# Kernel optimization log

Hardware: AMD Instinct MI355X
Metric: run time of the kernel (lower is better)

## Reference

```python
import jax, jax.numpy as jnp
import numpy as np
import math

N, T, NS, NO, HID = 256, 1000, 10, 10, 64


def gru_seq(x, Wi, Wh, bi, bh):
    # x: [N,T,D] -> hidden states [N,T,HID] (single-layer GRU, h0 = 0)
    xproj = x @ Wi + bi  # [N,T,3H], precompute input projections
    def step(h, xp):
        hp = h @ Wh + bh
        xr, xz, xn = jnp.split(xp, 3, axis=-1)
        hr, hz, hn = jnp.split(hp, 3, axis=-1)
        r = jax.nn.sigmoid(xr + hr)
        z = jax.nn.sigmoid(xz + hz)
        n = jnp.tanh(xn + r * hn)
        h_new = (1.0 - z) * n + z * h
        return h_new, h_new
    h0 = jnp.zeros((x.shape[0], Wh.shape[0]), x.dtype)
    _, hs = jax.lax.scan(step, h0, jnp.swapaxes(xproj, 0, 1))
    return jnp.swapaxes(hs, 0, 1)


def setup_inputs() -> dict:
    key = jax.random.key(0)
    ks = jax.random.split(key, 12)
    D = NO + NS  # GRU input = concat(y, x_hat)
    s = lambda fan: 1.0 / np.sqrt(fan)
    inp = {
        "Yi_batch": jax.random.normal(ks[0], (N, T, NO), jnp.float32),
        "X_hat_batch": jax.random.normal(ks[1], (N, T, NS), jnp.float32),
        # per-sample observation noise covariance: 0.5*I plus small random diagonal
        "Cw_batch": 0.5 * jnp.eye(NO, dtype=jnp.float32)[None] + jnp.eye(NO)[None] * 0.1 * jax.random.uniform(ks[2], (N, 1, 1), jnp.float32),
        "H": jax.random.normal(ks[3], (NO, NS), jnp.float32) * s(NS),
        "mu_w": jnp.zeros((NO, 1), jnp.float32),
        "Wi": jax.random.normal(ks[4], (D, 3 * HID), jnp.float32) * s(D),
        "Wh": jax.random.normal(ks[5], (HID, 3 * HID), jnp.float32) * s(HID),
        "bi": jnp.zeros((3 * HID,), jnp.float32),
        "bh": jnp.zeros((3 * HID,), jnp.float32),
        "W_mu": jax.random.normal(ks[6], (HID, NS), jnp.float32) * s(HID),
        "b_mu": jnp.zeros((NS,), jnp.float32),
        "W_var": jax.random.normal(ks[7], (HID, NS), jnp.float32) * s(HID),
        "b_var": jnp.zeros((NS,), jnp.float32),
    }
    return inp


def reference(Yi_batch, X_hat_batch, Cw_batch, H, mu_w, Wi, Wh, bi, bh, W_mu, b_mu, W_var, b_var):
    n_obs = Yi_batch.shape[-1]
    Tlen = Yi_batch.shape[1]
    # RNN: mu and (positive) vars per time step
    hs = gru_seq(jnp.concatenate([Yi_batch, X_hat_batch], axis=-1), Wi, Wh, bi, bh)
    mu_prev = hs @ W_mu + b_mu                       # [N,T,NS]
    var_prev = jax.nn.softplus(hs @ W_var + b_var)   # [N,T,NS] diag of L_xt_yt_prev
    # marginal over y: mu_y = H mu_prev + mu_w ; L_y = H diag(var) H^T + Cw
    mu_y = jnp.einsum('ij,ntj->nti', H, mu_prev) + mu_w[:, 0]
    HLH = jnp.einsum('ij,ntj,kj->ntik', H, var_prev, H)   # [N,T,NO,NO]
    L_y = HLH + Cw_batch[:, None]                          # broadcast Cw over time
    e = Yi_batch - mu_y
    # Gaussian log-likelihood via Cholesky (L_y is SPD)
    chol = jnp.linalg.cholesky(L_y)
    logdet = 2.0 * jnp.sum(jnp.log(jnp.diagonal(chol, axis1=-2, axis2=-1)), axis=-1)  # [N,T]
    sol = jnp.linalg.solve(L_y, e[..., None])[..., 0]
    quad = jnp.sum(e * sol, axis=-1)                       # [N,T]
    logprob = (-0.5 * n_obs * Tlen * math.log(2.0 * math.pi)
               - 0.5 * jnp.sum(logdet, axis=1)
               - 0.5 * jnp.sum(quad, axis=1))              # [N]
    return jnp.mean(logprob / (Tlen * n_obs))
```

## Files before the change

kernel.cpp:

```cpp
#include <hip/hip_runtime.h>
#include <math.h>

#define BN 256
#define TT 1000
#define NO 10
#define NS 10
#define HID 64
#define DIN 20
#define G3 192
#define WV 4
#define KW 16
#define GS 8
#define NG 125

__device__ __forceinline__ float bcast(float v, int l) {
    return __int_as_float(__builtin_amdgcn_readlane(__float_as_int(v), l));
}
__device__ __forceinline__ float rcpf(float x) { return __builtin_amdgcn_rcpf(x); }

__device__ __forceinline__ void sync_lds() {
    asm volatile("s_waitcnt lgkmcnt(0)\n\ts_barrier" ::: "memory");
}

__global__
__attribute__((amdgpu_flat_work_group_size(256, 256), amdgpu_waves_per_eu(1, 1)))
void gru_phase1(const float* __restrict__ Yi, const float* __restrict__ Xh,
                const float* __restrict__ Wi, const float* __restrict__ Wh,
                const float* __restrict__ bi, const float* __restrict__ bh,
                const float* __restrict__ Wmu, const float* __restrict__ Wvar,
                float* __restrict__ mv_out) {
    const int tid = threadIdx.x;
    const int lane = tid & 63;
    const int w = tid >> 6;
    const int kb = w * KW;

    __shared__ float4 part[2][WV][HID];
    __shared__ float pamv[2][WV][HID];
    __shared__ float inbuf[2][GS * DIN];
    __shared__ float obuf[2][GS * DIN];

    const int n = blockIdx.x;
    const float* ybase = Yi + (size_t)n * TT * NO;
    const float* xbase = Xh + (size_t)n * TT * NS;
    float* obase = mv_out + (size_t)n * TT * DIN;

    float whr[KW], whz[KW], whn[KW], wmv[KW];
    float wir[5], wiz[5], win[5];
#pragma unroll
    for (int k = 0; k < KW; ++k) {
        const int kk = kb + k;
        whr[k] = Wh[kk * G3 + lane];
        whz[k] = Wh[kk * G3 + 64 + lane];
        whn[k] = Wh[kk * G3 + 128 + lane];
        float wm = (lane < NS) ? Wmu[kk * NS + lane] : 0.0f;
        float wv = (lane >= NS && lane < 2 * NS) ? Wvar[kk * NS + (lane - NS)] : 0.0f;
        wmv[k] = wm + wv;
    }
#pragma unroll
    for (int k = 0; k < 5; ++k) {
        const int d = 5 * w + k;
        wir[k] = Wi[d * G3 + lane];
        wiz[k] = Wi[d * G3 + 64 + lane];
        win[k] = Wi[d * G3 + 128 + lane];
    }
    const float b_r  = bi[lane] + bh[lane];
    const float b_z  = bi[64 + lane] + bh[64 + lane];
    const float bx_n = bi[128 + lane];
    const float bh_n = bh[128 + lane];

    const int ibase = ((w >= 2) ? 80 : 0) + (w & 1) * 5;

    if (tid < 160)
        inbuf[0][tid] = (tid < 80) ? ybase[tid] : xbase[tid - 80];
    sync_lds();

    float h = 0.0f;

#pragma unroll 1
    for (int g = 0; g < NG; ++g) {
        float ld = 0.0f;
        const bool do_ld = (tid < 160) && (g + 1 < NG);
        if (do_ld)
            ld = (tid < 80) ? ybase[(size_t)(g + 1) * 80 + tid]
                            : xbase[(size_t)(g + 1) * 80 + (tid - 80)];
        const float* ib = inbuf[g & 1];

#pragma unroll
        for (int s = 0; s < GS; ++s) {
            const int ro = ibase + 10 * s;
            const float x0 = ib[ro], x1 = ib[ro + 1], x2 = ib[ro + 2];
            const float x3 = ib[ro + 3], x4 = ib[ro + 4];
            float pr = x0 * wir[0], pz = x0 * wiz[0], px = x0 * win[0];
            pr = fmaf(x1, wir[1], pr); pz = fmaf(x1, wiz[1], pz); px = fmaf(x1, win[1], px);
            pr = fmaf(x2, wir[2], pr); pz = fmaf(x2, wiz[2], pz); px = fmaf(x2, win[2], px);
            pr = fmaf(x3, wir[3], pr); pz = fmaf(x3, wiz[3], pz); px = fmaf(x3, win[3], px);
            pr = fmaf(x4, wir[4], pr); pz = fmaf(x4, wiz[4], pz); px = fmaf(x4, win[4], px);
            float pn = 0.0f, pm = 0.0f;
#pragma unroll
            for (int k = 0; k < KW; ++k) {
                float sv = bcast(h, kb + k);
                pr = fmaf(sv, whr[k], pr);
                pz = fmaf(sv, whz[k], pz);
                pn = fmaf(sv, whn[k], pn);
                pm = fmaf(sv, wmv[k], pm);
            }
            const int bufp = s & 1;
            part[bufp][w][lane] = make_float4(pr, pz, px, pn);
            pamv[bufp][w][lane] = pm;
            if (s == GS - 1 && do_ld) inbuf[(g + 1) & 1][tid] = ld;
            sync_lds();

            const float4 q0 = part[bufp][0][lane];
            const float4 q1 = part[bufp][1][lane];
            const float4 q2 = part[bufp][2][lane];
            const float4 q3 = part[bufp][3][lane];
            const float ar = b_r  + ((q0.x + q1.x) + (q2.x + q3.x));
            const float az = b_z  + ((q0.y + q1.y) + (q2.y + q3.y));
            const float ax = bx_n + ((q0.z + q1.z) + (q2.z + q3.z));
            const float ah = bh_n + ((q0.w + q1.w) + (q2.w + q3.w));
            if (w == 3) {
                float amv = (pamv[bufp][0][lane] + pamv[bufp][1][lane])
                          + (pamv[bufp][2][lane] + pamv[bufp][3][lane]);
                if (lane < DIN && !(g == 0 && s == 0)) {
                    const int tm1 = 8 * g + s - 1;
                    obuf[(tm1 >> 3) & 1][(tm1 & 7) * DIN + lane] = amv;
                }
            }
            if (s == 1 && g >= 1 && tid < 160)
                obase[(size_t)(g - 1) * 160 + tid] = obuf[(g - 1) & 1][tid];

            float r = rcpf(1.0f + __expf(-ar));
            float z = rcpf(1.0f + __expf(-az));
            float pre = fmaf(r, ah, ax);
            float e2 = __expf(2.0f * pre);
            float nn = 1.0f - 2.0f * rcpf(e2 + 1.0f);
            h = fmaf(z, h - nn, nn);
        }
    }

    {
        float pm = 0.0f;
#pragma unroll
        for (int k = 0; k < KW; ++k) pm = fmaf(bcast(h, kb + k), wmv[k], pm);
        pamv[0][w][lane] = pm;
        sync_lds();
        if (w == 3 && lane < DIN) {
            float amv = (pamv[0][0][lane] + pamv[0][1][lane])
                      + (pamv[0][2][lane] + pamv[0][3][lane]);
            obuf[0][7 * DIN + lane] = amv;
        }
        sync_lds();
        if (tid < 160)
            obase[(size_t)(NG - 1) * 160 + tid] = obuf[0][tid];
    }
}

__global__ void init_out(float* out) {
    out[0] = -0.918938533204672742f;
}

__global__ __launch_bounds__(256)
void lik_phase2(const float* __restrict__ Yi, const float* __restrict__ Cw,
                const float* __restrict__ Hm, const float* __restrict__ mu_w,
                const float* __restrict__ b_mu, const float* __restrict__ b_var,
                const float* __restrict__ mv_in, float* __restrict__ out) {
    __shared__ float sH[NO * NS];
    __shared__ float smw[NO], sbm[NS], sbv[NS];
    __shared__ float ssum[4];
    const int tid = threadIdx.x;
    if (tid < NO * NS) sH[tid] = Hm[tid];
    if (tid < NO) smw[tid] = mu_w[tid];
    if (tid < NS) { sbm[tid] = b_mu[tid]; sbv[tid] = b_var[tid]; }
    __syncthreads();

    const int gid = blockIdx.x * 256 + tid;
    float contrib = 0.0f;
    if (gid < BN * TT) {
        const int n = gid / TT;
        const float* mv = mv_in + (size_t)gid * DIN;
        float mu[NS], va[NS];
#pragma unroll
        for (int i = 0; i < NS; ++i) {
            mu[i] = mv[i] + sbm[i];
            float x = mv[NS + i] + sbv[i];
            va[i] = (x > 0.0f) ? (x + log1pf(__expf(-x))) : log1pf(__expf(x));
        }
        const float* y = Yi + (size_t)gid * NO;
        float e[NO];
#pragma unroll
        for (int i = 0; i < NO; ++i) {
            float m = smw[i];
#pragma unroll
            for (int j = 0; j < NS; ++j) m = fmaf(sH[i * NS + j], mu[j], m);
            e[i] = y[i] - m;
        }
        float M[NO][NO];
        const float* cw = Cw + (size_t)n * NO * NO;
#pragma unroll
        for (int i = 0; i < NO; ++i)
#pragma unroll
            for (int j = 0; j <= i; ++j) M[i][j] = cw[i * NO + j];
#pragma unroll
        for (int l = 0; l < NS; ++l) {
            float vl = va[l];
            float hv[NO];
#pragma unroll
            for (int i = 0; i < NO; ++i) hv[i] = sH[i * NS + l];
#pragma unroll
            for (int i = 0; i < NO; ++i) {
                float hvi = hv[i] * vl;
#pragma unroll
                for (int j = 0; j <= i; ++j) M[i][j] = fmaf(hvi, hv[j], M[i][j]);
            }
        }
        float logdet = 0.0f;
        float drs[NO];
#pragma unroll
        for (int j = 0; j < NO; ++j) {
            float d = M[j][j];
#pragma unroll
            for (int k = 0; k < j; ++k) d = fmaf(-M[j][k], M[j][k], d);
            logdet += __logf(d);
            float rs = __frsqrt_rn(d);
            drs[j] = rs;
            M[j][j] = d * rs;
#pragma unroll
            for (int i = j + 1; i < NO; ++i) {
                float v = M[i][j];
#pragma unroll
                for (int k = 0; k < j; ++k) v = fmaf(-M[i][k], M[j][k], v);
                M[i][j] = v * rs;
            }
        }
        float wv[NO];
        float quad = 0.0f;
#pragma unroll
        for (int i = 0; i < NO; ++i) {
            float v = e[i];
#pragma unroll
            for (int k = 0; k < i; ++k) v = fmaf(-M[i][k], wv[k], v);
            wv[i] = v * drs[i] * rcpf(M[i][i] * drs[i]);
            quad = fmaf(wv[i], wv[i], quad);
        }
        const float SCALE = 0.5f / ((float)BN * (float)TT * (float)NO);
        contrib = -(logdet + quad) * SCALE;
    }

#pragma unroll
    for (int off = 32; off > 0; off >>= 1) contrib += __shfl_down(contrib, off);
    if ((tid & 63) == 0) ssum[tid >> 6] = contrib;
    __syncthreads();
    if (tid == 0) {
        float s = ssum[0] + ssum[1] + ssum[2] + ssum[3];
        atomicAdd(out, s);
    }
}

extern "C" void kernel_launch(void* const* d_in, const int* in_sizes, int n_in,
                              void* d_out, int out_size, void* d_ws, size_t ws_size,
                              hipStream_t stream) {
    const float* Yi    = (const float*)d_in[0];
    const float* Xh    = (const float*)d_in[1];
    const float* Cw    = (const float*)d_in[2];
    const float* Hm    = (const float*)d_in[3];
    const float* mu_w  = (const float*)d_in[4];
    const float* Wi    = (const float*)d_in[5];
    const float* Wh    = (const float*)d_in[6];
    const float* bi    = (const float*)d_in[7];
    const float* bh    = (const float*)d_in[8];
    const float* W_mu  = (const float*)d_in[9];
    const float* b_mu  = (const float*)d_in[10];
    const float* W_var = (const float*)d_in[11];
    const float* b_var = (const float*)d_in[12];
    float* out = (float*)d_out;
    float* mv  = (float*)d_ws;

    init_out<<<1, 1, 0, stream>>>(out);
    gru_phase1<<<dim3(BN), dim3(256), 0, stream>>>(Yi, Xh, Wi, Wh, bi, bh,
                                                   W_mu, W_var, mv);
    lik_phase2<<<dim3((BN * TT + 255) / 256), dim3(256), 0, stream>>>(
        Yi, Cw, Hm, mu_w, b_mu, b_var, mv, out);
}
```

Baseline: 593.6 us.

## Run each GRU sample on a single wavefront with full hidden weights in registers

Replaces the four-wave-per-sample GRU kernel with one 64-lane wave per sample. Each wave holds all 64 recurrent weight rows plus the input weights in registers, so the per-step cross-wave LDS reduction and workgroup barrier go away. Inputs are staged through a per-wave LDS buffer in a padded interleaved layout, and outputs are written straight to global memory each step. In exchange each wave does four times the FMAs and readlanes per step on one SIMD, and register pressure rises to roughly 320 VGPRs.

Measured after the change: 1.064 ms. 1.79x slower.

```diff
diff --git a/kernel.cpp b/kernel.cpp
--- a/kernel.cpp
+++ b/kernel.cpp
@@ -8,8 +8,6 @@
 #define HID 64
 #define DIN 20
 #define G3 192
-#define WV 4
-#define KW 16
 #define GS 8
 #define NG 125
 
@@ -18,140 +16,112 @@
 }
 __device__ __forceinline__ float rcpf(float x) { return __builtin_amdgcn_rcpf(x); }
 
-__device__ __forceinline__ void sync_lds() {
-    asm volatile("s_waitcnt lgkmcnt(0)\n\ts_barrier" ::: "memory");
-}
-
 __global__
-__attribute__((amdgpu_flat_work_group_size(256, 256), amdgpu_waves_per_eu(1, 1)))
-void gru_phase1(const float* __restrict__ Yi, const float* __restrict__ Xh,
-                const float* __restrict__ Wi, const float* __restrict__ Wh,
-                const float* __restrict__ bi, const float* __restrict__ bh,
-                const float* __restrict__ Wmu, const float* __restrict__ Wvar,
-                float* __restrict__ mv_out) {
-    const int tid = threadIdx.x;
-    const int lane = tid & 63;
-    const int w = tid >> 6;
-    const int kb = w * KW;
-
-    __shared__ float4 part[2][WV][HID];
-    __shared__ float pamv[2][WV][HID];
-    __shared__ float inbuf[2][GS * DIN];
-    __shared__ float obuf[2][GS * DIN];
-
+__attribute__((amdgpu_flat_work_group_size(64, 64), amdgpu_waves_per_eu(1, 1)))
+void gru_onewave(const float* __restrict__ Yi, const float* __restrict__ Xh,
+                 const float* __restrict__ Wi, const float* __restrict__ Wh,
+                 const float* __restrict__ bi, const float* __restrict__ bh,
+                 const float* __restrict__ Wmu, const float* __restrict__ Wvar,
+                 float* __restrict__ mv_out) {
+    const int lane = threadIdx.x;
     const int n = blockIdx.x;
-    const float* ybase = Yi + (size_t)n * TT * NO;
-    const float* xbase = Xh + (size_t)n * TT * NS;
-    float* obase = mv_out + (size_t)n * TT * DIN;
-
-    float whr[KW], whz[KW], whn[KW], wmv[KW];
-    float wir[5], wiz[5], win[5];
-#pragma unroll
-    for (int k = 0; k < KW; ++k) {
-        const int kk = kb + k;
-        whr[k] = Wh[kk * G3 + lane];
-        whz[k] = Wh[kk * G3 + 64 + lane];
-        whn[k] = Wh[kk * G3 + 128 + lane];
-        float wm = (lane < NS) ? Wmu[kk * NS + lane] : 0.0f;
-        float wv = (lane >= NS && lane < 2 * NS) ? Wvar[kk * NS + (lane - NS)] : 0.0f;
-        wmv[k] = wm + wv;
-    }
-#pragma unroll
-    for (int k = 0; k < 5; ++k) {
-        const int d = 5 * w + k;
-        wir[k] = Wi[d * G3 + lane];
-        wiz[k] = Wi[d * G3 + 64 + lane];
-        win[k] = Wi[d * G3 + 128 + lane];
-    }
-    const float b_r  = bi[lane] + bh[lane];
-    const float b_z  = bi[64 + lane] + bh[64 + lane];
-    const float bx_n = bi[128 + lane];
-    const float bh_n = bh[128 + lane];
-
-    const int ibase = ((w >= 2) ? 80 : 0) + (w & 1) * 5;
-
-    if (tid < 160)
-        inbuf[0][tid] = (tid < 80) ? ybase[tid] : xbase[tid - 80];
-    sync_lds();
+
+    __shared__ __align__(16) float inb[2][GS * 32];
+
+    float whr[HID], whz[HID], whn[HID], wmv[HID];
+#pragma unroll
+    for (int k = 0; k < HID; ++k) {
+        whr[k] = Wh[k * G3 + lane];
+        whz[k] = Wh[k * G3 + 64 + lane];
+        whn[k] = Wh[k * G3 + 128 + lane];
+        float wm = 0.0f;
+        if (lane < NS) wm = Wmu[k * NS + lane];
+        else if (lane < DIN) wm = Wvar[k * NS + (lane - NS)];
+        wmv[k] = wm;
+    }
+    float wir[DIN], wiz[DIN], win[DIN];
+#pragma unroll
+    for (int d = 0; d < DIN; ++d) {
+        wir[d] = Wi[d * G3 + lane];
+        wiz[d] = Wi[d * G3 + 64 + lane];
+        win[d] = Wi[d * G3 + 128 + lane];
+    }
+    const float b_r = bi[lane] + bh[lane];
+    const float b_z = bi[64 + lane] + bh[64 + lane];
+    const float bxn = bi[128 + lane];
+    const float bhn = bh[128 + lane];
+
+    const float* yb = Yi + (size_t)n * TT * NO;
+    const float* xb = Xh + (size_t)n * TT * NS;
+    float* ob = mv_out + (size_t)n * TT * DIN;
+
+    const int s0 = lane / 10, j0 = lane - 10 * s0;
+    const int s1 = (64 + lane) / 10, j1 = (64 + lane) - 10 * s1;
+    const int wy0 = s0 * 32 + j0, wx0 = wy0 + 10;
+    const int wy1 = s1 * 32 + j1, wx1 = wy1 + 10;
+
+    float ly0 = yb[lane], lx0 = xb[lane];
+    float ly1 = 0.0f, lx1 = 0.0f;
+    if (lane < 16) { ly1 = yb[64 + lane]; lx1 = xb[64 + lane]; }
 
     float h = 0.0f;
 
 #pragma unroll 1
     for (int g = 0; g < NG; ++g) {
-        float ld = 0.0f;
-        const bool do_ld = (tid < 160) && (g + 1 < NG);
-        if (do_ld)
-            ld = (tid < 80) ? ybase[(size_t)(g + 1) * 80 + tid]
-                            : xbase[(size_t)(g + 1) * 80 + (tid - 80)];
-        const float* ib = inbuf[g & 1];
-
-#pragma unroll
+        float* buf = inb[g & 1];
+        buf[wy0] = ly0; buf[wx0] = lx0;
+        if (lane < 16) { buf[wy1] = ly1; buf[wx1] = lx1; }
+        if (g + 1 < NG) {
+            const size_t o = (size_t)(g + 1) * (GS * NO);
+            ly0 = yb[o + lane]; lx0 = xb[o + lane];
+            if (lane < 16) { ly1 = yb[o + 64 + lane]; lx1 = xb[o + 64 + lane]; }
+        }
+
+#pragma unroll 2
         for (int s = 0; s < GS; ++s) {
-            const int ro = ibase + 10 * s;
-            const float x0 = ib[ro], x1 = ib[ro + 1], x2 = ib[ro + 2];
-            const float x3 = ib[ro + 3], x4 = ib[ro + 4];
-            float pr = x0 * wir[0], pz = x0 * wiz[0], px = x0 * win[0];
-            pr = fmaf(x1, wir[1], pr); pz = fmaf(x1, wiz[1], pz); px = fmaf(x1, win[1], px);
-            pr = fmaf(x2, wir[2], pr); pz = fmaf(x2, wiz[2], pz); px = fmaf(x2, win[2], px);
-            pr = fmaf(x3, wir[3], pr); pz = fmaf(x3, wiz[3], pz); px = fmaf(x3, win[3], px);
-            pr = fmaf(x4, wir[4], pr); pz = fmaf(x4, wiz[4], pz); px = fmaf(x4, win[4], px);
-            float pn = 0.0f, pm = 0.0f;
-#pragma unroll
-            for (int k = 0; k < KW; ++k) {
-                float sv = bcast(h, kb + k);
-                pr = fmaf(sv, whr[k], pr);
-                pz = fmaf(sv, whz[k], pz);
-                pn = fmaf(sv, whn[k], pn);
-                pm = fmaf(sv, wmv[k], pm);
+            const float4* qp = (const float4*)(buf + s * 32);
+            const float4 q0 = qp[0], q1 = qp[1], q2 = qp[2], q3 = qp[3], q4 = qp[4];
+
+            float ar = b_r, az = b_z, ax = bxn, ah = bhn, am = 0.0f;
+
+#pragma unroll
+            for (int k = 0; k < HID; ++k) {
+                const float hv = bcast(h, k);
+                ar = fmaf(hv, whr[k], ar);
+                az = fmaf(hv, whz[k], az);
+                ah = fmaf(hv, whn[k], ah);
+                am = fmaf(hv, wmv[k], am);
             }
-            const int bufp = s & 1;
-            part[bufp][w][lane] = make_float4(pr, pz, px, pn);
-            pamv[bufp][w][lane] = pm;
-            if (s == GS - 1 && do_ld) inbuf[(g + 1) & 1][tid] = ld;
-            sync_lds();
-
-            const float4 q0 = part[bufp][0][lane];
-            const float4 q1 = part[bufp][1][lane];
-            const float4 q2 = part[bufp][2][lane];
-            const float4 q3 = part[bufp][3][lane];
-            const float ar = b_r  + ((q0.x + q1.x) + (q2.x + q3.x));
-            const float az = b_z  + ((q0.y + q1.y) + (q2.y + q3.y));
-            const float ax = bx_n + ((q0.z + q1.z) + (q2.z + q3.z));
-            const float ah = bh_n + ((q0.w + q1.w) + (q2.w + q3.w));
-            if (w == 3) {
-                float amv = (pamv[bufp][0][lane] + pamv[bufp][1][lane])
-                          + (pamv[bufp][2][lane] + pamv[bufp][3][lane]);
-                if (lane < DIN && !(g == 0 && s == 0)) {
-                    const int tm1 = 8 * g + s - 1;
-                    obuf[(tm1 >> 3) & 1][(tm1 & 7) * DIN + lane] = amv;
-                }
-            }
-            if (s == 1 && g >= 1 && tid < 160)
-                obase[(size_t)(g - 1) * 160 + tid] = obuf[(g - 1) & 1][tid];
-
-            float r = rcpf(1.0f + __expf(-ar));
-            float z = rcpf(1.0f + __expf(-az));
-            float pre = fmaf(r, ah, ax);
-            float e2 = __expf(2.0f * pre);
-            float nn = 1.0f - 2.0f * rcpf(e2 + 1.0f);
+
+#define IN3(d, val) { const float xv_ = (val);              \
+            ar = fmaf(xv_, wir[d], ar);                     \
+            az = fmaf(xv_, wiz[d], az);                     \
+            ax = fmaf(xv_, win[d], ax); }
+            IN3(0,  q0.x) IN3(1,  q0.y) IN3(2,  q0.z) IN3(3,  q0.w)
+            IN3(4,  q1.x) IN3(5,  q1.y) IN3(6,  q1.z) IN3(7,  q1.w)
+            IN3(8,  q2.x) IN3(9,  q2.y)
+            IN3(10, q2.z) IN3(11, q2.w)
+            IN3(12, q3.x) IN3(13, q3.y) IN3(14, q3.z) IN3(15, q3.w)
+            IN3(16, q4.x) IN3(17, q4.y) IN3(18, q4.z) IN3(19, q4.w)
+#undef IN3
+
+            const int t = g * GS + s;
+            if (t > 0 && lane < DIN) ob[(size_t)(t - 1) * DIN + lane] = am;
+
+            const float r = rcpf(1.0f + __expf(-ar));
+            const float z = rcpf(1.0f + __expf(-az));
+            const float pre = fmaf(r, ah, ax);
+            const float e2 = __expf(2.0f * pre);
+            const float nn = 1.0f - 2.0f * rcpf(e2 + 1.0f);
             h = fmaf(z, h - nn, nn);
         }
     }
 
     {
-        float pm = 0.0f;
-#pragma unroll
-        for (int k = 0; k < KW; ++k) pm = fmaf(bcast(h, kb + k), wmv[k], pm);
-        pamv[0][w][lane] = pm;
-        sync_lds();
-        if (w == 3 && lane < DIN) {
-            float amv = (pamv[0][0][lane] + pamv[0][1][lane])
-                      + (pamv[0][2][lane] + pamv[0][3][lane]);
-            obuf[0][7 * DIN + lane] = amv;
-        }
-        sync_lds();
-        if (tid < 160)
-            obase[(size_t)(NG - 1) * 160 + tid] = obuf[0][tid];
+        float am = 0.0f;
+#pragma unroll
+        for (int k = 0; k < HID; ++k) am = fmaf(bcast(h, k), wmv[k], am);
+        if (lane < DIN) ob[(size_t)(TT - 1) * DIN + lane] = am;
     }
 }
 
@@ -276,7 +246,7 @@
     float* mv  = (float*)d_ws;
 
     init_out<<<1, 1, 0, stream>>>(out);
-    gru_phase1<<<dim3(BN), dim3(256), 0, stream>>>(Yi, Xh, Wi, Wh, bi, bh,
+    gru_onewave<<<dim3(BN), dim3(64), 0, stream>>>(Yi, Xh, Wi, Wh, bi, bh,
                                                    W_mu, W_var, mv);
     lik_phase2<<<dim3((BN * TT + 255) / 256), dim3(256), 0, stream>>>(
         Yi, Cw, Hm, mu_w, b_mu, b_var, mv, out);
```

## Pack two GRU sequences per 512-thread workgroup in phase one

Applied to the files above, without the earlier changes.

Each workgroup now runs two independent batch samples as two 256-thread groups, with per-group shared buffers. The grid is halved to 128 blocks and the occupancy hint moves to two waves per EU. The aim is to hide the serial recurrence's latency by interleaving two sequences' waves on each SIMD. The cost is that only half the CUs are used, the two sequences share one barrier and so are lock-stepped, and each wave gets less issue bandwidth.

Result: slower. 801.6 us (+35.0%).

```diff
diff --git a/kernel.cpp b/kernel.cpp
--- a/kernel.cpp
+++ b/kernel.cpp
@@ -12,6 +12,7 @@
 #define KW 16
 #define GS 8
 #define NG 125
+#define SPB 2
 
 __device__ __forceinline__ float bcast(float v, int l) {
     return __int_as_float(__builtin_amdgcn_readlane(__float_as_int(v), l));
@@ -23,29 +24,30 @@
 }
 
 __global__
-__attribute__((amdgpu_flat_work_group_size(256, 256), amdgpu_waves_per_eu(1, 1)))
+__attribute__((amdgpu_flat_work_group_size(512, 512), amdgpu_waves_per_eu(2, 2)))
 void gru_phase1(const float* __restrict__ Yi, const float* __restrict__ Xh,
                 const float* __restrict__ Wi, const float* __restrict__ Wh,
                 const float* __restrict__ bi, const float* __restrict__ bh,
                 const float* __restrict__ Wmu, const float* __restrict__ Wvar,
                 float* __restrict__ mv_out) {
-    const int tid = threadIdx.x;
-    const int lane = tid & 63;
-    const int w = tid >> 6;
+    const int tid  = threadIdx.x;
+    const int grp  = tid >> 8;
+    const int tidg = tid & 255;
+    const int lane = tidg & 63;
+    const int w = tidg >> 6;
     const int kb = w * KW;
 
-    __shared__ float4 part[2][WV][HID];
-    __shared__ float pamv[2][WV][HID];
-    __shared__ float inbuf[2][GS * DIN];
-    __shared__ float obuf[2][GS * DIN];
-
-    const int n = blockIdx.x;
+    __shared__ float4 part[SPB][2][WV][HID];
+    __shared__ float pamv[SPB][2][WV][HID];
+    __shared__ float inbuf[SPB][2][GS * DIN];
+    __shared__ float obuf[SPB][2][GS * DIN];
+
+    const int n = blockIdx.x * SPB + grp;
     const float* ybase = Yi + (size_t)n * TT * NO;
     const float* xbase = Xh + (size_t)n * TT * NS;
     float* obase = mv_out + (size_t)n * TT * DIN;
 
     float whr[KW], whz[KW], whn[KW], wmv[KW];
-    float wir[5], wiz[5], win[5];
 #pragma unroll
     for (int k = 0; k < KW; ++k) {
         const int kk = kb + k;
@@ -56,6 +58,7 @@
         float wv = (lane >= NS && lane < 2 * NS) ? Wvar[kk * NS + (lane - NS)] : 0.0f;
         wmv[k] = wm + wv;
     }
+    float wir[5], wiz[5], win[5];
 #pragma unroll
     for (int k = 0; k < 5; ++k) {
         const int d = 5 * w + k;
@@ -70,8 +73,8 @@
 
     const int ibase = ((w >= 2) ? 80 : 0) + (w & 1) * 5;
 
-    if (tid < 160)
-        inbuf[0][tid] = (tid < 80) ? ybase[tid] : xbase[tid - 80];
+    if (tidg < 160)
+        inbuf[grp][0][tidg] = (tidg < 80) ? ybase[tidg] : xbase[tidg - 80];
     sync_lds();
 
     float h = 0.0f;
@@ -79,11 +82,11 @@
 #pragma unroll 1
     for (int g = 0; g < NG; ++g) {
         float ld = 0.0f;
-        const bool do_ld = (tid < 160) && (g + 1 < NG);
+        const bool do_ld = (tidg < 160) && (g + 1 < NG);
         if (do_ld)
-            ld = (tid < 80) ? ybase[(size_t)(g + 1) * 80 + tid]
-                            : xbase[(size_t)(g + 1) * 80 + (tid - 80)];
-        const float* ib = inbuf[g & 1];
+            ld = (tidg < 80) ? ybase[(size_t)(g + 1) * 80 + tidg]
+                             : xbase[(size_t)(g + 1) * 80 + (tidg - 80)];
+        const float* ib = inbuf[grp][g & 1];
 
 #pragma unroll
         for (int s = 0; s < GS; ++s) {
@@ -105,29 +108,29 @@
                 pm = fmaf(sv, wmv[k], pm);
             }
             const int bufp = s & 1;
-            part[bufp][w][lane] = make_float4(pr, pz, px, pn);
-            pamv[bufp][w][lane] = pm;
-            if (s == GS - 1 && do_ld) inbuf[(g + 1) & 1][tid] = ld;
+            part[grp][bufp][w][lane] = make_float4(pr, pz, px, pn);
+            pamv[grp][bufp][w][lane] = pm;
+            if (s == GS - 1 && do_ld) inbuf[grp][(g + 1) & 1][tidg] = ld;
             sync_lds();
 
-            const float4 q0 = part[bufp][0][lane];
-            const float4 q1 = part[bufp][1][lane];
-            const float4 q2 = part[bufp][2][lane];
-            const float4 q3 = part[bufp][3][lane];
+            const float4 q0 = part[grp][bufp][0][lane];
+            const float4 q1 = part[grp][bufp][1][lane];
+            const float4 q2 = part[grp][bufp][2][lane];
+            const float4 q3 = part[grp][bufp][3][lane];
             const float ar = b_r  + ((q0.x + q1.x) + (q2.x + q3.x));
             const float az = b_z  + ((q0.y + q1.y) + (q2.y + q3.y));
             const float ax = bx_n + ((q0.z + q1.z) + (q2.z + q3.z));
             const float ah = bh_n + ((q0.w + q1.w) + (q2.w + q3.w));
             if (w == 3) {
-                float amv = (pamv[bufp][0][lane] + pamv[bufp][1][lane])
-                          + (pamv[bufp][2][lane] + pamv[bufp][3][lane]);
+                float amv = (pamv[grp][bufp][0][lane] + pamv[grp][bufp][1][lane])
+                          + (pamv[grp][bufp][2][lane] + pamv[grp][bufp][3][lane]);
                 if (lane < DIN && !(g == 0 && s == 0)) {
                     const int tm1 = 8 * g + s - 1;
-                    obuf[(tm1 >> 3) & 1][(tm1 & 7) * DIN + lane] = amv;
+                    obuf[grp][(tm1 >> 3) & 1][(tm1 & 7) * DIN + lane] = amv;
                 }
             }
-            if (s == 1 && g >= 1 && tid < 160)
-                obase[(size_t)(g - 1) * 160 + tid] = obuf[(g - 1) & 1][tid];
+            if (s == 1 && g >= 1 && tidg < 160)
+                obase[(size_t)(g - 1) * 160 + tidg] = obuf[grp][(g - 1) & 1][tidg];
 
             float r = rcpf(1.0f + __expf(-ar));
             float z = rcpf(1.0f + __expf(-az));
@@ -142,16 +145,16 @@
         float pm = 0.0f;
 #pragma unroll
         for (int k = 0; k < KW; ++k) pm = fmaf(bcast(h, kb + k), wmv[k], pm);
-        pamv[0][w][lane] = pm;
+        pamv[grp][0][w][lane] = pm;
         sync_lds();
         if (w == 3 && lane < DIN) {
-            float amv = (pamv[0][0][lane] + pamv[0][1][lane])
-                      + (pamv[0][2][lane] + pamv[0][3][lane]);
-            obuf[0][7 * DIN + lane] = amv;
+            float amv = (pamv[grp][0][0][lane] + pamv[grp][0][1][lane])
+                      + (pamv[grp][0][2][lane] + pamv[grp][0][3][lane]);
+            obuf[grp][0][7 * DIN + lane] = amv;
         }
         sync_lds();
-        if (tid < 160)
-            obase[(size_t)(NG - 1) * 160 + tid] = obuf[0][tid];
+        if (tidg < 160)
+            obase[(size_t)(NG - 1) * 160 + tidg] = obuf[grp][0][tidg];
     }
 }
 
@@ -276,8 +279,8 @@
     float* mv  = (float*)d_ws;
 
     init_out<<<1, 1, 0, stream>>>(out);
-    gru_phase1<<<dim3(BN), dim3(256), 0, stream>>>(Yi, Xh, Wi, Wh, bi, bh,
-                                                   W_mu, W_var, mv);
+    gru_phase1<<<dim3(BN / SPB), dim3(512), 0, stream>>>(Yi, Xh, Wi, Wh, bi, bh,
+                                                         W_mu, W_var, mv);
     lik_phase2<<<dim3((BN * TT + 255) / 256), dim3(256), 0, stream>>>(
         Yi, Cw, Hm, mu_w, b_mu, b_var, mv, out);
 }
```
